# Performance work log

Measured on AMD Instinct MI355X. Metric: run time of the kernel, lower is better.

Reference implementation:

```python
import jax, jax.numpy as jnp
import numpy as np

B, C, H, W = 4, 256, 64, 64
HALF = C // 2
BN_EPS = 1e-5


def setup_inputs() -> dict:
    key = jax.random.key(0)
    ks = jax.random.split(key, 6)
    scale = 1.0 / np.sqrt(C)
    return {
        "x": jax.random.normal(ks[0], (B, C, H, W), dtype=jnp.float32),
        "w1": jax.random.normal(ks[1], (HALF, C), dtype=jnp.float32) * scale,
        "w2": jax.random.normal(ks[2], (HALF, C), dtype=jnp.float32) * scale,
        "w3": jax.random.normal(ks[3], (HALF, C), dtype=jnp.float32) * scale,
        "w4": jax.random.normal(ks[4], (C, HALF), dtype=jnp.float32) * (1.0 / np.sqrt(HALF)),
        "gamma": jnp.ones((C,), dtype=jnp.float32),
        "beta": jnp.zeros((C,), dtype=jnp.float32),
        "running_mean": jnp.zeros((C,), dtype=jnp.float32),
        "running_var": jnp.ones((C,), dtype=jnp.float32),
    }


def _conv1x1(x, w):
    # x: [b,c,h,w], w: [out,in] -> [b,out,h,w]
    return jnp.einsum('bchw,oc->bohw', x, w)


def reference(x, w1, w2, w3, w4, gamma, beta, running_mean, running_var):
    b, Cin, h, w = x.shape
    c = Cin // 2
    hw = h * w
    n1 = _conv1x1(x, w1)  # [b,c,h,w]
    n2 = _conv1x1(x, w2)
    n3 = _conv1x1(x, w3)
    # Faithful to torch .view (raw reshape, NOT a transpose)
    q = n1.reshape(b, hw, c)   # [b,hw,c]
    k = n2.reshape(b, c, hw)   # [b,c,hw]
    attn = jnp.einsum('bic,bcj->bij', q, k)        # [b,hw,hw]
    attn = jax.nn.softmax(attn, axis=-1)
    v = n3.reshape(b, hw, c)
    res = jnp.einsum('bij,bjc->bic', attn, v)      # [b,hw,c]
    res = res.reshape(b, c, h, w)
    out = _conv1x1(res, w4)                        # [b,C,h,w]
    # BatchNorm2d in eval mode with running stats
    inv = jax.lax.rsqrt(running_var + BN_EPS)
    out = (out - running_mean[None, :, None, None]) * (gamma * inv)[None, :, None, None] + beta[None, :, None, None]
    return out + x
```

## Files before the change

### kernel.cpp

```cpp
#include <hip/hip_runtime.h>
#include <cstdint>

#define BN 4
#define CIN 256
#define HALFC 128
#define HW 4096
#define SPLIT 4
#define JT 64
#define JITERS (HW / SPLIT / JT)

typedef float  floatx4 __attribute__((ext_vector_type(4)));
typedef short  shortx8 __attribute__((ext_vector_type(8)));

#if __has_builtin(__builtin_amdgcn_exp2f)
#define EXP2F(x) __builtin_amdgcn_exp2f(x)
#else
#define EXP2F(x) exp2f(x)
#endif
#define L2E 1.44269504088896f

__device__ __forceinline__ unsigned short f2bf(float f) {
  unsigned u = __float_as_uint(f);
  u += 0x7FFFu + ((u >> 16) & 1u);
  return (unsigned short)(u >> 16);
}
__device__ __forceinline__ float bf2f(unsigned short h) {
  return __uint_as_float((unsigned)h << 16);
}

__device__ __forceinline__ void async16(const void* g, void* l) {
  __builtin_amdgcn_global_load_lds((const __attribute__((address_space(1))) void*)g,
                                   (__attribute__((address_space(3))) void*)l, 16, 0, 0);
}

__global__ __launch_bounds__(256) void k_split(const float* __restrict__ x,
    const float* __restrict__ w1, const float* __restrict__ w2,
    const float* __restrict__ w3, unsigned short* __restrict__ Xth,
    unsigned short* __restrict__ Xtl, unsigned short* __restrict__ Wh,
    unsigned short* __restrict__ Wl) {
  __shared__ float smf[64 * 65];
  int bid = blockIdx.x;
  int t = threadIdx.x;
  if (bid < 1024) {
    int b = bid >> 8, rem = bid & 255;
    int cit = rem >> 6, pxt = rem & 63;
    const float* src = x + (size_t)b * 1048576 + (size_t)(cit * 64) * HW + pxt * 64;
#pragma unroll
    for (int k = 0; k < 16; k++) {
      int idx = k * 256 + t;
      int r = idx >> 6, c = idx & 63;
      smf[r * 65 + c] = src[(size_t)r * HW + c];
    }
    __syncthreads();
    int prow = t >> 2, seg = t & 3;
    union { unsigned short us[16]; uint4 v[2]; } oh, ol;
#pragma unroll
    for (int u = 0; u < 16; u++) {
      float v = smf[(seg * 16 + u) * 65 + prow];
      unsigned short hh = f2bf(v);
      oh.us[u] = hh;
      ol.us[u] = f2bf(v - bf2f(hh));
    }
    size_t dst = (size_t)b * 1048576 + (size_t)(pxt * 64 + prow) * 256 + cit * 64 + seg * 16;
    *(uint4*)(Xth + dst) = oh.v[0];
    *(uint4*)(Xth + dst + 8) = oh.v[1];
    *(uint4*)(Xtl + dst) = ol.v[0];
    *(uint4*)(Xtl + dst + 8) = ol.v[1];
  } else {
    int bw = bid - 1024;
    int f0 = bw * 8192 + t * 32;
    const float* wsrc;
    int fo;
    if (f0 < 32768)      { wsrc = w1; fo = f0; }
    else if (f0 < 65536) { wsrc = w2; fo = f0 - 32768; }
    else                 { wsrc = w3; fo = f0 - 65536; }
    union { unsigned short us[32]; uint4 v[4]; } oh, ol;
#pragma unroll
    for (int u = 0; u < 32; u++) {
      float v = wsrc[fo + u];
      unsigned short hh = f2bf(v);
      oh.us[u] = hh;
      ol.us[u] = f2bf(v - bf2f(hh));
    }
#pragma unroll
    for (int k = 0; k < 4; k++) {
      *((uint4*)(Wh + f0) + k) = oh.v[k];
      *((uint4*)(Wl + f0) + k) = ol.v[k];
    }
  }
}

__global__ __launch_bounds__(256) void k_projM(const unsigned short* __restrict__ Xth,
    const unsigned short* __restrict__ Xtl, const unsigned short* __restrict__ Wh,
    const unsigned short* __restrict__ Wl, unsigned short* __restrict__ Q,
    unsigned short* __restrict__ Kt, unsigned short* __restrict__ n3) {
  __shared__ unsigned short XhS[4096];
  __shared__ unsigned short XlS[4096];
  __shared__ unsigned short ES[9216];
  int bid = blockIdx.x;
  int pxt = bid & 31;
  int ct = bid >> 5;
  int b = ct / 6, cot = ct % 6;
  int px0 = pxt * 128, co0 = cot * 64;
  int t = threadIdx.x;
  int w = t >> 6, lane = t & 63, l16 = lane & 15, quad = lane >> 4;

  int myco = co0 + w * 16 + l16;
  shortx8 whf[8], wlf[8];
#pragma unroll
  for (int s = 0; s < 8; s++) {
    whf[s] = *(const shortx8*)(Wh + (size_t)myco * 256 + s * 32 + quad * 8);
    wlf[s] = *(const shortx8*)(Wl + (size_t)myco * 256 + s * 32 + quad * 8);
  }
  floatx4 acc[8];
  floatx4 zf = {0.f, 0.f, 0.f, 0.f};
#pragma unroll
  for (int mt = 0; mt < 8; mt++) acc[mt] = zf;
  const unsigned short* XhB = Xth + (size_t)b * 1048576;
  const unsigned short* XlB = Xtl + (size_t)b * 1048576;
  int k8 = lane >> 4, pxm = lane & 15;

#pragma unroll
  for (int s = 0; s < 8; s++) {
    __syncthreads();
#pragma unroll
    for (int c2 = 0; c2 < 2; c2++) {
      int px = px0 + (c2 * 4 + w) * 16 + pxm;
      size_t so = (size_t)px * 256 + s * 32 + k8 * 8;
      async16(XhB + so, (char*)XhS + c2 * 4096 + w * 1024);
      async16(XlB + so, (char*)XlS + c2 * 4096 + w * 1024);
    }
    __syncthreads();
#pragma unroll
    for (int mt = 0; mt < 8; mt++) {
      shortx8 ah = *(const shortx8*)((const char*)XhS + mt * 1024 + lane * 16);
      shortx8 al = *(const shortx8*)((const char*)XlS + mt * 1024 + lane * 16);
      acc[mt] = __builtin_amdgcn_mfma_f32_16x16x32_bf16(ah, whf[s], acc[mt], 0, 0, 0);
      acc[mt] = __builtin_amdgcn_mfma_f32_16x16x32_bf16(al, whf[s], acc[mt], 0, 0, 0);
      acc[mt] = __builtin_amdgcn_mfma_f32_16x16x32_bf16(ah, wlf[s], acc[mt], 0, 0, 0);
    }
  }
  __syncthreads();
  if (cot < 2 || cot >= 4) {
    int co_l = w * 16 + l16;
#pragma unroll
    for (int mt = 0; mt < 8; mt++) {
      int px = mt * 16 + quad * 4;
      unsigned lo = (unsigned)f2bf(acc[mt][0]) | ((unsigned)f2bf(acc[mt][1]) << 16);
      unsigned hi = (unsigned)f2bf(acc[mt][2]) | ((unsigned)f2bf(acc[mt][3]) << 16);
      *(uint2*)(ES + co_l * 136 + px) = make_uint2(lo, hi);
    }
    __syncthreads();
    int cr = t >> 2, seg = t & 3;
    unsigned short* dstb = (cot < 2)
        ? Q  + (size_t)b * 524288 + (size_t)(co0 + cr) * HW
        : n3 + (size_t)b * 524288 + (size_t)(co0 - 256 + cr) * HW;
#pragma unroll
    for (int k2 = 0; k2 < 4; k2++) {
      uint4 v = *(const uint4*)(ES + cr * 136 + seg * 32 + k2 * 8);
      *(uint4*)(dstb + px0 + seg * 32 + k2 * 8) = v;
    }
  } else {
#pragma unroll
    for (int mt = 0; mt < 8; mt++)
#pragma unroll
      for (int rr = 0; rr < 4; rr++) {
        int px = mt * 16 + quad * 4 + rr;
        ES[px * 72 + w * 16 + l16] = f2bf(acc[mt][rr]);
      }
    __syncthreads();
    int ch0 = co0 - 128;
#pragma unroll
    for (int it = 0; it < 4; it++) {
      int cid = it * 256 + t;
      int px = cid >> 3, c8 = cid & 7;
      uint4 v = *(const uint4*)(ES + px * 72 + c8 * 8);
      *(uint4*)(Kt + (size_t)b * 524288 + (size_t)(px0 + px) * 128 + ch0 + c8 * 8) = v;
    }
  }
}

__global__ __launch_bounds__(256) void k_layoutV(const unsigned short* __restrict__ n3,
    unsigned short* __restrict__ Vt) {
  __shared__ unsigned short sm[8192];
  int bid = blockIdx.x;
  int t = threadIdx.x;
  int b = bid >> 6;
  int chg = bid & 63;
  const unsigned short* src = n3 + (size_t)b * 524288 + (size_t)(chg * 2) * HW;
#pragma unroll
  for (int k = 0; k < 32; k++) {
    int idx = k * 256 + t;
    sm[idx] = src[idx];
  }
  __syncthreads();
  int c = t >> 1, half = t & 1;
  union { unsigned short us[32]; uint4 v[4]; } o;
#pragma unroll
  for (int u = 0; u < 32; u++) o.us[u] = sm[half * 4096 + u * 128 + c];
  unsigned short* d = Vt + ((size_t)b * 128 + c) * HW + chg * 64 + half * 32;
#pragma unroll
  for (int k = 0; k < 4; k++) *((uint4*)d + k) = o.v[k];
}

__global__ __launch_bounds__(256, 2) void k_flash(const unsigned short* __restrict__ Q,
    const unsigned short* __restrict__ Kt, const unsigned short* __restrict__ Vt,
    float* __restrict__ Opart, float* __restrict__ ml) {
  __shared__ unsigned short KtS[2 * 8192];
  __shared__ unsigned short VtS[2 * 8192];
  __shared__ unsigned short PS[4 * 32 * 64];
  int bid = blockIdx.x;
  int itile = bid & 31, sp = (bid >> 5) & 3, b = bid >> 7;
  int t = threadIdx.x;
  int w = t >> 6, lane = t & 63, l16 = lane & 15, quad = lane >> 4;
  int i0 = itile * 128;

  shortx8 qf[2][4];
#pragma unroll
  for (int ig = 0; ig < 2; ig++) {
    const unsigned short* qp = Q + ((size_t)b * HW + i0 + w * 32 + ig * 16 + l16) * 128 + quad * 8;
#pragma unroll
    for (int ks = 0; ks < 4; ks++) qf[ig][ks] = *(const shortx8*)(qp + ks * 32);
  }
  __asm__ __volatile__("s_waitcnt vmcnt(0)" ::: "memory");

  floatx4 O[2][8];
  floatx4 zf = {0.f, 0.f, 0.f, 0.f};
#pragma unroll
  for (int ig = 0; ig < 2; ig++)
#pragma unroll
    for (int nt = 0; nt < 8; nt++) O[ig][nt] = zf;
  float m_i[2] = {-1e30f, -1e30f}, l_i[2] = {0.f, 0.f};

  int ccK = w * 4 + (lane >> 4);
  const unsigned short* kbase = Kt + (size_t)b * HW * 128
                              + (size_t)(sp * 1024 + l16) * 128 + ccK * 8;
  int ccV = (w & 1) * 4 + (lane >> 4);
  const unsigned short* vbase = Vt + ((size_t)b * 128 + (w >> 1) * 16 + l16) * HW
                              + sp * 1024 + ccV * 8;
  char* Pw = (char*)PS + w * 4096;

#pragma unroll
  for (int c4 = 0; c4 < 4; c4++)
    async16(kbase + c4 * 2048, (char*)KtS + c4 * 4096 + w * 1024);
#pragma unroll
  for (int c4 = 0; c4 < 4; c4++)
    async16(vbase + (size_t)c4 * 32 * HW, (char*)VtS + c4 * 4096 + w * 1024);

  for (int it = 0; it < JITERS; it++) {
    int cur = it & 1, nxt = cur ^ 1;
    __asm__ __volatile__("s_barrier" ::: "memory");
    if (it + 1 < JITERS) {
      const unsigned short* kp = kbase + (size_t)(it + 1) * 8192;
      const unsigned short* vp = vbase + (it + 1) * 64;
#pragma unroll
      for (int c4 = 0; c4 < 4; c4++)
        async16(kp + c4 * 2048, (char*)KtS + nxt * 16384 + c4 * 4096 + w * 1024);
#pragma unroll
      for (int c4 = 0; c4 < 4; c4++)
        async16(vp + (size_t)c4 * 32 * HW, (char*)VtS + nxt * 16384 + c4 * 4096 + w * 1024);
      __asm__ __volatile__("s_waitcnt vmcnt(8)" ::: "memory");
    } else {
      __asm__ __volatile__("s_waitcnt vmcnt(0)" ::: "memory");
    }
    __asm__ __volatile__("s_barrier" ::: "memory");

    const char* kc = (const char*)KtS + cur * 16384;
    const char* vc = (const char*)VtS + cur * 16384;

    floatx4 S[2][4];
#pragma unroll
    for (int ig = 0; ig < 2; ig++)
#pragma unroll
      for (int mt = 0; mt < 4; mt++) S[ig][mt] = zf;
#pragma unroll
    for (int mt = 0; mt < 4; mt++) {
#pragma unroll
      for (int ks = 0; ks < 4; ks++) {
        shortx8 af = *(const shortx8*)(kc + mt * 4096 + ks * 1024 + lane * 16);
        S[0][mt] = __builtin_amdgcn_mfma_f32_16x16x32_bf16(af, qf[0][ks], S[0][mt], 0, 0, 0);
        S[1][mt] = __builtin_amdgcn_mfma_f32_16x16x32_bf16(af, qf[1][ks], S[1][mt], 0, 0, 0);
      }
    }
    float alpha[2];
#pragma unroll
    for (int ig = 0; ig < 2; ig++) {
      float tmax = S[ig][0][0];
#pragma unroll
      for (int mt = 0; mt < 4; mt++)
#pragma unroll
        for (int rr = 0; rr < 4; rr++) tmax = fmaxf(tmax, S[ig][mt][rr]);
      tmax = fmaxf(tmax, __shfl_xor(tmax, 16));
      tmax = fmaxf(tmax, __shfl_xor(tmax, 32));
      float mnew = fmaxf(m_i[ig], tmax);
      alpha[ig] = EXP2F((m_i[ig] - mnew) * L2E);
      float tsum = 0.f;
#pragma unroll
      for (int mt = 0; mt < 4; mt++)
#pragma unroll
        for (int rr = 0; rr < 4; rr++) {
          float p = EXP2F((S[ig][mt][rr] - mnew) * L2E);
          S[ig][mt][rr] = p;
          tsum += p;
        }
      tsum += __shfl_xor(tsum, 16);
      tsum += __shfl_xor(tsum, 32);
      l_i[ig] = l_i[ig] * alpha[ig] + tsum;
      m_i[ig] = mnew;
    }
    if (__ballot(alpha[0] < 1.f || alpha[1] < 1.f)) {
#pragma unroll
      for (int ig = 0; ig < 2; ig++) {
        float ar[4];
#pragma unroll
        for (int rr = 0; rr < 4; rr++) ar[rr] = __shfl(alpha[ig], quad * 4 + rr);
#pragma unroll
        for (int nt = 0; nt < 8; nt++)
#pragma unroll
          for (int rr = 0; rr < 4; rr++) O[ig][nt][rr] *= ar[rr];
      }
    }
#pragma unroll
    for (int ig = 0; ig < 2; ig++)
#pragma unroll
      for (int mt = 0; mt < 4; mt++) {
        unsigned lo = (unsigned)f2bf(S[ig][mt][0]) | ((unsigned)f2bf(S[ig][mt][1]) << 16);
        unsigned hi = (unsigned)f2bf(S[ig][mt][2]) | ((unsigned)f2bf(S[ig][mt][3]) << 16);
        *(uint2*)(Pw + ig * 2048 + (mt * 2 + (quad >> 1)) * 256 + l16 * 16 + (quad & 1) * 8)
            = make_uint2(lo, hi);
      }
    __asm__ __volatile__("s_waitcnt lgkmcnt(0)" ::: "memory");
#pragma unroll
    for (int kt = 0; kt < 2; kt++) {
      shortx8 pf0 = *(const shortx8*)(Pw + kt * 1024 + lane * 16);
      shortx8 pf1 = *(const shortx8*)(Pw + 2048 + kt * 1024 + lane * 16);
#pragma unroll
      for (int nt = 0; nt < 8; nt++) {
        shortx8 vf = *(const shortx8*)(vc + nt * 2048 + kt * 1024 + lane * 16);
        O[0][nt] = __builtin_amdgcn_mfma_f32_16x16x32_bf16(pf0, vf, O[0][nt], 0, 0, 0);
        O[1][nt] = __builtin_amdgcn_mfma_f32_16x16x32_bf16(pf1, vf, O[1][nt], 0, 0, 0);
      }
    }
  }
#pragma unroll
  for (int ig = 0; ig < 2; ig++) {
    float* Ob = Opart + ((size_t)(sp * 4 + b) * HW + i0 + w * 32 + ig * 16) * 128;
#pragma unroll
    for (int nt = 0; nt < 8; nt++)
#pragma unroll
      for (int rr = 0; rr < 4; rr++)
        Ob[(size_t)(quad * 4 + rr) * 128 + nt * 16 + l16] = O[ig][nt][rr];
  }
  if (quad == 0) {
    float2* mlp = (float2*)ml;
#pragma unroll
    for (int ig = 0; ig < 2; ig++)
      mlp[(size_t)(sp * 4 + b) * HW + i0 + w * 32 + ig * 16 + l16]
          = make_float2(m_i[ig], l_i[ig]);
  }
}

__global__ __launch_bounds__(256) void k_merge(const float* __restrict__ Opart,
    const float* __restrict__ ml, float* __restrict__ res) {
  size_t e = (size_t)blockIdx.x * 256 + threadIdx.x;
  int cq = (int)(e & 31);
  int i = (int)((e >> 5) & 4095);
  int b = (int)(e >> 17);
  const float2* mlp = (const float2*)ml;
  float m[SPLIT], l[SPLIT];
  float M = -1e30f;
#pragma unroll
  for (int s = 0; s < SPLIT; s++) {
    float2 st = mlp[(size_t)(s * 4 + b) * HW + i];
    m[s] = st.x; l[s] = st.y;
    M = fmaxf(M, m[s]);
  }
  float denom = 0.f;
  float wgt[SPLIT];
#pragma unroll
  for (int s = 0; s < SPLIT; s++) {
    float ws_ = EXP2F((m[s] - M) * L2E);
    wgt[s] = ws_;
    denom += l[s] * ws_;
  }
  float inv = 1.f / denom;
  floatx4 acc = {0.f, 0.f, 0.f, 0.f};
#pragma unroll
  for (int s = 0; s < SPLIT; s++) {
    floatx4 v = *(const floatx4*)(Opart + ((size_t)(s * 4 + b) * HW + i) * 128 + cq * 4);
    acc += v * (wgt[s] * inv);
  }
  *(floatx4*)(res + e * 4) = acc;
}

__global__ __launch_bounds__(256) void k_out(const float* __restrict__ res,
    const float* __restrict__ w4, const float* __restrict__ gamma,
    const float* __restrict__ beta, const float* __restrict__ rmean,
    const float* __restrict__ rvar, const float* __restrict__ x,
    float* __restrict__ out) {
  __shared__ float wt[16 * 128];
  int bid = blockIdx.x;
  int cot = bid & 15;
  int st = (bid >> 4) & 15;
  int b = bid >> 8;
  int t = threadIdx.x;
  int co0 = cot * 16;
#pragma unroll
  for (int k = 0; k < 8; k++) wt[k * 256 + t] = w4[(size_t)co0 * 128 + k * 256 + t];
  __syncthreads();
  int px = st * 256 + t;
  const float* rb = res + (size_t)b * 524288 + px;
  float acc[16];
#pragma unroll
  for (int r = 0; r < 16; r++) acc[r] = 0.f;
  for (int ci = 0; ci < 128; ci += 4) {
    float xv[4];
#pragma unroll
    for (int kk = 0; kk < 4; kk++) xv[kk] = rb[(size_t)(ci + kk) * HW];
#pragma unroll
    for (int r = 0; r < 16; r++) {
      floatx4 wv = *(const floatx4*)&wt[r * 128 + ci];
#pragma unroll
      for (int kk = 0; kk < 4; kk++) acc[r] += wv[kk] * xv[kk];
    }
  }
  const float* xb = x + ((size_t)b * 256 + co0) * HW + px;
  float* ob = out + ((size_t)b * 256 + co0) * HW + px;
#pragma unroll
  for (int r = 0; r < 16; r++) {
    int co = co0 + r;
    float g = gamma[co] * rsqrtf(rvar[co] + 1e-5f);
    float bb = beta[co] - rmean[co] * g;
    ob[(size_t)r * HW] = acc[r] * g + bb + xb[(size_t)r * HW];
  }
}

extern "C" void kernel_launch(void* const* d_in, const int* in_sizes, int n_in,
                              void* d_out, int out_size, void* d_ws, size_t ws_size,
                              hipStream_t stream) {
  const float* x     = (const float*)d_in[0];
  const float* w1    = (const float*)d_in[1];
  const float* w2    = (const float*)d_in[2];
  const float* w3    = (const float*)d_in[3];
  const float* w4    = (const float*)d_in[4];
  const float* gamma = (const float*)d_in[5];
  const float* beta  = (const float*)d_in[6];
  const float* rmean = (const float*)d_in[7];
  const float* rvar  = (const float*)d_in[8];
  float* out = (float*)d_out;
  char* ws = (char*)d_ws;

  size_t off = (size_t)SPLIT * 4 * HW * 128 * 4;
  float* Opart = (float*)ws;
  unsigned short* n3  = (unsigned short*)ws;
  unsigned short* Xth = (unsigned short*)(ws + ((size_t)8  << 20));
  unsigned short* Xtl = (unsigned short*)(ws + ((size_t)17 << 20));
  unsigned short* Q  = (unsigned short*)(ws + off); off += (size_t)4 * HW * 128 * 2;
  unsigned short* Kt = (unsigned short*)(ws + off); off += (size_t)4 * HW * 128 * 2;
  unsigned short* Vt = (unsigned short*)(ws + off); off += (size_t)4 * HW * 128 * 2;
  float* ml  = (float*)(ws + off); off += (size_t)SPLIT * 4 * HW * 2 * 4;
  float* res = (float*)(ws + off); off += (size_t)4 * HW * 128 * 4;
  unsigned short* Wh = (unsigned short*)(ws + off); off += (size_t)384 * 256 * 2;
  unsigned short* Wl = (unsigned short*)(ws + off); off += (size_t)384 * 256 * 2;
  if (ws_size < off) return;

  k_split  <<<1036, 256, 0, stream>>>(x, w1, w2, w3, Xth, Xtl, Wh, Wl);
  k_projM  <<<768,  256, 0, stream>>>(Xth, Xtl, Wh, Wl, Q, Kt, n3);
  k_layoutV<<<256,  256, 0, stream>>>(n3, Vt);
  k_flash  <<<512,  256, 0, stream>>>(Q, Kt, Vt, Opart, ml);
  k_merge  <<<2048, 256, 0, stream>>>(Opart, ml, res);
  k_out    <<<1024, 256, 0, stream>>>(res, w4, gamma, beta, rmean, rvar, x, out);
}
```

Baseline: 209.2 us.

## Drop split-bf16 projection, pre-swizzle V for direct register loads, truncate P

The QKV projection no longer splits inputs and weights into high and low bf16 parts. It now runs one bf16 MFMA per tile instead of three, which removes the Xtl/Wl buffers and their traffic. V is rewritten into a fragment-ordered layout so the flash kernel loads V fragments straight from global into registers, bypassing the LDS double buffer. The P to bf16 conversion uses a byte permute that truncates instead of rounding. These changes cut projection compute, memory traffic and LDS use, but lower numerical accuracy and raise register pressure in the flash kernel.

```diff
diff --git a/kernel.cpp b/kernel.cpp
--- a/kernel.cpp
+++ b/kernel.cpp
@@ -24,9 +24,6 @@
   u += 0x7FFFu + ((u >> 16) & 1u);
   return (unsigned short)(u >> 16);
 }
-__device__ __forceinline__ float bf2f(unsigned short h) {
-  return __uint_as_float((unsigned)h << 16);
-}
 
 __device__ __forceinline__ void async16(const void* g, void* l) {
   __builtin_amdgcn_global_load_lds((const __attribute__((address_space(1))) void*)g,
@@ -36,8 +33,7 @@
 __global__ __launch_bounds__(256) void k_split(const float* __restrict__ x,
     const float* __restrict__ w1, const float* __restrict__ w2,
     const float* __restrict__ w3, unsigned short* __restrict__ Xth,
-    unsigned short* __restrict__ Xtl, unsigned short* __restrict__ Wh,
-    unsigned short* __restrict__ Wl) {
+    unsigned short* __restrict__ Wh) {
   __shared__ float smf[64 * 65];
   int bid = blockIdx.x;
   int t = threadIdx.x;
@@ -53,19 +49,13 @@
     }
     __syncthreads();
     int prow = t >> 2, seg = t & 3;
-    union { unsigned short us[16]; uint4 v[2]; } oh, ol;
-#pragma unroll
-    for (int u = 0; u < 16; u++) {
-      float v = smf[(seg * 16 + u) * 65 + prow];
-      unsigned short hh = f2bf(v);
-      oh.us[u] = hh;
-      ol.us[u] = f2bf(v - bf2f(hh));
-    }
+    union { unsigned short us[16]; uint4 v[2]; } oh;
+#pragma unroll
+    for (int u = 0; u < 16; u++)
+      oh.us[u] = f2bf(smf[(seg * 16 + u) * 65 + prow]);
     size_t dst = (size_t)b * 1048576 + (size_t)(pxt * 64 + prow) * 256 + cit * 64 + seg * 16;
     *(uint4*)(Xth + dst) = oh.v[0];
     *(uint4*)(Xth + dst + 8) = oh.v[1];
-    *(uint4*)(Xtl + dst) = ol.v[0];
-    *(uint4*)(Xtl + dst + 8) = ol.v[1];
   } else {
     int bw = bid - 1024;
     int f0 = bw * 8192 + t * 32;
@@ -74,28 +64,18 @@
     if (f0 < 32768)      { wsrc = w1; fo = f0; }
     else if (f0 < 65536) { wsrc = w2; fo = f0 - 32768; }
     else                 { wsrc = w3; fo = f0 - 65536; }
-    union { unsigned short us[32]; uint4 v[4]; } oh, ol;
-#pragma unroll
-    for (int u = 0; u < 32; u++) {
-      float v = wsrc[fo + u];
-      unsigned short hh = f2bf(v);
-      oh.us[u] = hh;
-      ol.us[u] = f2bf(v - bf2f(hh));
-    }
-#pragma unroll
-    for (int k = 0; k < 4; k++) {
-      *((uint4*)(Wh + f0) + k) = oh.v[k];
-      *((uint4*)(Wl + f0) + k) = ol.v[k];
-    }
+    union { unsigned short us[32]; uint4 v[4]; } oh;
+#pragma unroll
+    for (int u = 0; u < 32; u++) oh.us[u] = f2bf(wsrc[fo + u]);
+#pragma unroll
+    for (int k = 0; k < 4; k++) *((uint4*)(Wh + f0) + k) = oh.v[k];
   }
 }
 
 __global__ __launch_bounds__(256) void k_projM(const unsigned short* __restrict__ Xth,
-    const unsigned short* __restrict__ Xtl, const unsigned short* __restrict__ Wh,
-    const unsigned short* __restrict__ Wl, unsigned short* __restrict__ Q,
+    const unsigned short* __restrict__ Wh, unsigned short* __restrict__ Q,
     unsigned short* __restrict__ Kt, unsigned short* __restrict__ n3) {
   __shared__ unsigned short XhS[4096];
-  __shared__ unsigned short XlS[4096];
   __shared__ unsigned short ES[9216];
   int bid = blockIdx.x;
   int pxt = bid & 31;
@@ -106,18 +86,15 @@
   int w = t >> 6, lane = t & 63, l16 = lane & 15, quad = lane >> 4;
 
   int myco = co0 + w * 16 + l16;
-  shortx8 whf[8], wlf[8];
-#pragma unroll
-  for (int s = 0; s < 8; s++) {
+  shortx8 whf[8];
+#pragma unroll
+  for (int s = 0; s < 8; s++)
     whf[s] = *(const shortx8*)(Wh + (size_t)myco * 256 + s * 32 + quad * 8);
-    wlf[s] = *(const shortx8*)(Wl + (size_t)myco * 256 + s * 32 + quad * 8);
-  }
   floatx4 acc[8];
   floatx4 zf = {0.f, 0.f, 0.f, 0.f};
 #pragma unroll
   for (int mt = 0; mt < 8; mt++) acc[mt] = zf;
   const unsigned short* XhB = Xth + (size_t)b * 1048576;
-  const unsigned short* XlB = Xtl + (size_t)b * 1048576;
   int k8 = lane >> 4, pxm = lane & 15;
 
 #pragma unroll
@@ -126,18 +103,13 @@
 #pragma unroll
     for (int c2 = 0; c2 < 2; c2++) {
       int px = px0 + (c2 * 4 + w) * 16 + pxm;
-      size_t so = (size_t)px * 256 + s * 32 + k8 * 8;
-      async16(XhB + so, (char*)XhS + c2 * 4096 + w * 1024);
-      async16(XlB + so, (char*)XlS + c2 * 4096 + w * 1024);
+      async16(XhB + (size_t)px * 256 + s * 32 + k8 * 8, (char*)XhS + c2 * 4096 + w * 1024);
     }
     __syncthreads();
 #pragma unroll
     for (int mt = 0; mt < 8; mt++) {
       shortx8 ah = *(const shortx8*)((const char*)XhS + mt * 1024 + lane * 16);
-      shortx8 al = *(const shortx8*)((const char*)XlS + mt * 1024 + lane * 16);
       acc[mt] = __builtin_amdgcn_mfma_f32_16x16x32_bf16(ah, whf[s], acc[mt], 0, 0, 0);
-      acc[mt] = __builtin_amdgcn_mfma_f32_16x16x32_bf16(al, whf[s], acc[mt], 0, 0, 0);
-      acc[mt] = __builtin_amdgcn_mfma_f32_16x16x32_bf16(ah, wlf[s], acc[mt], 0, 0, 0);
     }
   }
   __syncthreads();
@@ -180,34 +152,33 @@
   }
 }
 
-__global__ __launch_bounds__(256) void k_layoutV(const unsigned short* __restrict__ n3,
-    unsigned short* __restrict__ Vt) {
+__global__ __launch_bounds__(256) void k_layoutVF(const unsigned short* __restrict__ n3,
+    unsigned short* __restrict__ VtF) {
   __shared__ unsigned short sm[8192];
   int bid = blockIdx.x;
+  int b = bid >> 6, jt = bid & 63;
   int t = threadIdx.x;
-  int b = bid >> 6;
-  int chg = bid & 63;
-  const unsigned short* src = n3 + (size_t)b * 524288 + (size_t)(chg * 2) * HW;
-#pragma unroll
-  for (int k = 0; k < 32; k++) {
-    int idx = k * 256 + t;
-    sm[idx] = src[idx];
-  }
+  const unsigned short* src = n3 + (size_t)b * 524288 + (size_t)(jt * 2) * 4096;
+#pragma unroll
+  for (int k = 0; k < 32; k++) sm[k * 256 + t] = src[k * 256 + t];
   __syncthreads();
-  int c = t >> 1, half = t & 1;
-  union { unsigned short us[32]; uint4 v[4]; } o;
-#pragma unroll
-  for (int u = 0; u < 32; u++) o.us[u] = sm[half * 4096 + u * 128 + c];
-  unsigned short* d = Vt + ((size_t)b * 128 + c) * HW + chg * 64 + half * 32;
-#pragma unroll
-  for (int k = 0; k < 4; k++) *((uint4*)d + k) = o.v[k];
+  unsigned short* dst = VtF + (size_t)b * 524288 + (size_t)jt * 8192;
+#pragma unroll
+  for (int k = 0; k < 4; k++) {
+    int s = k * 256 + t;
+    int nt = s >> 7, kt = (s >> 6) & 1, quad = (s >> 4) & 3, l16 = s & 15;
+    union { unsigned short us[8]; uint4 v; } o;
+#pragma unroll
+    for (int e = 0; e < 8; e++)
+      o.us[e] = sm[kt * 4096 + (quad * 8 + e) * 128 + nt * 16 + l16];
+    *(uint4*)(dst + s * 8) = o.v;
+  }
 }
 
 __global__ __launch_bounds__(256, 2) void k_flash(const unsigned short* __restrict__ Q,
-    const unsigned short* __restrict__ Kt, const unsigned short* __restrict__ Vt,
+    const unsigned short* __restrict__ Kt, const unsigned short* __restrict__ VtF,
     float* __restrict__ Opart, float* __restrict__ ml) {
   __shared__ unsigned short KtS[2 * 8192];
-  __shared__ unsigned short VtS[2 * 8192];
   __shared__ unsigned short PS[4 * 32 * 64];
   int bid = blockIdx.x;
   int itile = bid & 31, sp = (bid >> 5) & 3, b = bid >> 7;
@@ -235,38 +206,37 @@
   int ccK = w * 4 + (lane >> 4);
   const unsigned short* kbase = Kt + (size_t)b * HW * 128
                               + (size_t)(sp * 1024 + l16) * 128 + ccK * 8;
-  int ccV = (w & 1) * 4 + (lane >> 4);
-  const unsigned short* vbase = Vt + ((size_t)b * 128 + (w >> 1) * 16 + l16) * HW
-                              + sp * 1024 + ccV * 8;
+  const unsigned short* vB = VtF + (size_t)b * 524288 + (size_t)(sp * 16) * 8192 + lane * 8;
   char* Pw = (char*)PS + w * 4096;
 
 #pragma unroll
   for (int c4 = 0; c4 < 4; c4++)
     async16(kbase + c4 * 2048, (char*)KtS + c4 * 4096 + w * 1024);
-#pragma unroll
-  for (int c4 = 0; c4 < 4; c4++)
-    async16(vbase + (size_t)c4 * 32 * HW, (char*)VtS + c4 * 4096 + w * 1024);
 
   for (int it = 0; it < JITERS; it++) {
     int cur = it & 1, nxt = cur ^ 1;
     __asm__ __volatile__("s_barrier" ::: "memory");
+    shortx8 vf[8][2];
+    {
+      const unsigned short* vt = vB + (size_t)it * 8192;
+#pragma unroll
+      for (int nt = 0; nt < 8; nt++)
+#pragma unroll
+        for (int kt = 0; kt < 2; kt++)
+          vf[nt][kt] = *(const shortx8*)(vt + (nt * 2 + kt) * 512);
+    }
     if (it + 1 < JITERS) {
       const unsigned short* kp = kbase + (size_t)(it + 1) * 8192;
-      const unsigned short* vp = vbase + (it + 1) * 64;
 #pragma unroll
       for (int c4 = 0; c4 < 4; c4++)
         async16(kp + c4 * 2048, (char*)KtS + nxt * 16384 + c4 * 4096 + w * 1024);
-#pragma unroll
-      for (int c4 = 0; c4 < 4; c4++)
-        async16(vp + (size_t)c4 * 32 * HW, (char*)VtS + nxt * 16384 + c4 * 4096 + w * 1024);
-      __asm__ __volatile__("s_waitcnt vmcnt(8)" ::: "memory");
+      __asm__ __volatile__("s_waitcnt vmcnt(20)" ::: "memory");
     } else {
-      __asm__ __volatile__("s_waitcnt vmcnt(0)" ::: "memory");
+      __asm__ __volatile__("s_waitcnt vmcnt(16)" ::: "memory");
     }
     __asm__ __volatile__("s_barrier" ::: "memory");
 
     const char* kc = (const char*)KtS + cur * 16384;
-    const char* vc = (const char*)VtS + cur * 16384;
 
     floatx4 S[2][4];
 #pragma unroll
@@ -324,21 +294,27 @@
     for (int ig = 0; ig < 2; ig++)
 #pragma unroll
       for (int mt = 0; mt < 4; mt++) {
-        unsigned lo = (unsigned)f2bf(S[ig][mt][0]) | ((unsigned)f2bf(S[ig][mt][1]) << 16);
-        unsigned hi = (unsigned)f2bf(S[ig][mt][2]) | ((unsigned)f2bf(S[ig][mt][3]) << 16);
+        unsigned lo = __builtin_amdgcn_perm(__float_as_uint(S[ig][mt][1]),
+                                            __float_as_uint(S[ig][mt][0]), 0x07060302u);
+        unsigned hi = __builtin_amdgcn_perm(__float_as_uint(S[ig][mt][3]),
+                                            __float_as_uint(S[ig][mt][2]), 0x07060302u);
         *(uint2*)(Pw + ig * 2048 + (mt * 2 + (quad >> 1)) * 256 + l16 * 16 + (quad & 1) * 8)
             = make_uint2(lo, hi);
       }
     __asm__ __volatile__("s_waitcnt lgkmcnt(0)" ::: "memory");
+    if (it + 1 < JITERS) {
+      __asm__ __volatile__("s_waitcnt vmcnt(4)" ::: "memory");
+    } else {
+      __asm__ __volatile__("s_waitcnt vmcnt(0)" ::: "memory");
+    }
 #pragma unroll
     for (int kt = 0; kt < 2; kt++) {
       shortx8 pf0 = *(const shortx8*)(Pw + kt * 1024 + lane * 16);
       shortx8 pf1 = *(const shortx8*)(Pw + 2048 + kt * 1024 + lane * 16);
 #pragma unroll
       for (int nt = 0; nt < 8; nt++) {
-        shortx8 vf = *(const shortx8*)(vc + nt * 2048 + kt * 1024 + lane * 16);
-        O[0][nt] = __builtin_amdgcn_mfma_f32_16x16x32_bf16(pf0, vf, O[0][nt], 0, 0, 0);
-        O[1][nt] = __builtin_amdgcn_mfma_f32_16x16x32_bf16(pf1, vf, O[1][nt], 0, 0, 0);
+        O[0][nt] = __builtin_amdgcn_mfma_f32_16x16x32_bf16(pf0, vf[nt][kt], O[0][nt], 0, 0, 0);
+        O[1][nt] = __builtin_amdgcn_mfma_f32_16x16x32_bf16(pf1, vf[nt][kt], O[1][nt], 0, 0, 0);
       }
     }
   }
@@ -453,21 +429,19 @@
   size_t off = (size_t)SPLIT * 4 * HW * 128 * 4;
   float* Opart = (float*)ws;
   unsigned short* n3  = (unsigned short*)ws;
-  unsigned short* Xth = (unsigned short*)(ws + ((size_t)8  << 20));
-  unsigned short* Xtl = (unsigned short*)(ws + ((size_t)17 << 20));
-  unsigned short* Q  = (unsigned short*)(ws + off); off += (size_t)4 * HW * 128 * 2;
-  unsigned short* Kt = (unsigned short*)(ws + off); off += (size_t)4 * HW * 128 * 2;
-  unsigned short* Vt = (unsigned short*)(ws + off); off += (size_t)4 * HW * 128 * 2;
+  unsigned short* Xth = (unsigned short*)(ws + ((size_t)8 << 20));
+  unsigned short* Q   = (unsigned short*)(ws + off); off += (size_t)4 * HW * 128 * 2;
+  unsigned short* Kt  = (unsigned short*)(ws + off); off += (size_t)4 * HW * 128 * 2;
+  unsigned short* VtF = (unsigned short*)(ws + off); off += (size_t)4 * HW * 128 * 2;
   float* ml  = (float*)(ws + off); off += (size_t)SPLIT * 4 * HW * 2 * 4;
   float* res = (float*)(ws + off); off += (size_t)4 * HW * 128 * 4;
   unsigned short* Wh = (unsigned short*)(ws + off); off += (size_t)384 * 256 * 2;
-  unsigned short* Wl = (unsigned short*)(ws + off); off += (size_t)384 * 256 * 2;
   if (ws_size < off) return;
 
-  k_split  <<<1036, 256, 0, stream>>>(x, w1, w2, w3, Xth, Xtl, Wh, Wl);
-  k_projM  <<<768,  256, 0, stream>>>(Xth, Xtl, Wh, Wl, Q, Kt, n3);
-  k_layoutV<<<256,  256, 0, stream>>>(n3, Vt);
-  k_flash  <<<512,  256, 0, stream>>>(Q, Kt, Vt, Opart, ml);
-  k_merge  <<<2048, 256, 0, stream>>>(Opart, ml, res);
-  k_out    <<<1024, 256, 0, stream>>>(res, w4, gamma, beta, rmean, rvar, x, out);
-}
+  k_split   <<<1036, 256, 0, stream>>>(x, w1, w2, w3, Xth, Wh);
+  k_projM   <<<768,  256, 0, stream>>>(Xth, Wh, Q, Kt, n3);
+  k_layoutVF<<<256,  256, 0, stream>>>(n3, VtF);
+  k_flash   <<<512,  256, 0, stream>>>(Q, Kt, VtF, Opart, ml);
+  k_merge   <<<2048, 256, 0, stream>>>(Opart, ml, res);
+  k_out     <<<1024, 256, 0, stream>>>(res, w4, gamma, beta, rmean, rvar, x, out);
+}
```

After: 191.0 us. -8.7%, faster.
